# Kernel tuning notes

Hardware: AMD Instinct MI355X
Metric: run time of the kernel (lower is better)

## Reference

```python
import jax, jax.numpy as jnp
import numpy as np

SEQ, BATCH, DIM = 2048, 32, 1024


def setup_inputs() -> dict:
    key = jax.random.key(0)
    k1, k2, k3, k4, k5 = jax.random.split(key, 5)
    scale = 1.0 / np.sqrt(DIM)
    return {
        "decoder_hidden": jax.random.normal(k1, (BATCH, 1, DIM), dtype=jnp.float32),
        "encoder_out": jax.random.normal(k2, (SEQ, BATCH, DIM), dtype=jnp.float32),
        "W_enc": jax.random.normal(k3, (DIM, DIM), dtype=jnp.float32) * scale,
        "W_dec": jax.random.normal(k4, (DIM, DIM), dtype=jnp.float32) * scale,
        "V_att": jax.random.normal(k5, (1, DIM), dtype=jnp.float32) * scale,
    }


def reference(decoder_hidden, encoder_out, W_enc, W_dec, V_att):
    # encoder_out: (seq, batch, dim); decoder_hidden: (batch, 1, dim)
    # torch Linear: y = x @ W.T with W of shape (out, in)
    keys = jnp.einsum('sbd,ed->bse', encoder_out, W_enc)      # (batch, seq, dim)
    query = decoder_hidden @ W_dec.T                           # (batch, 1, dim)
    scores = jnp.tanh(keys + query)                            # (batch, seq, dim)
    logits = jnp.einsum('bsd,d->bs', scores, V_att[0])         # (batch, seq)
    alpha = jax.nn.softmax(logits, axis=1)[..., None]          # (batch, seq, 1)
    # context = alpha^T @ encoder_out_permuted -> (batch, 1, dim)
    context = jnp.einsum('bs,sbd->bd', alpha[..., 0], encoder_out)[:, None, :]
    return context, jnp.transpose(alpha, (2, 0, 1))            # (1, batch, seq)
```

## Files before the change

### kernel.cpp

```cpp
#include <hip/hip_runtime.h>
#include <hip/hip_bf16.h>
#include <math.h>

#define SEQ   2048
#define BATCH 32
#define DIM   1024
#define MROWS (SEQ*BATCH)
#define NT2   4
#define NCH   16
#define NKT   16

typedef __attribute__((ext_vector_type(8))) short short8;
typedef __attribute__((ext_vector_type(8))) unsigned short u16x8;
typedef __attribute__((ext_vector_type(4))) float f32x4;

__device__ __forceinline__ unsigned short f2bf(float f) {
  unsigned u = __builtin_bit_cast(unsigned, f);
  u += 0x7FFFu + ((u >> 16) & 1u);
  return (unsigned short)(u >> 16);
}

__device__ __forceinline__ void gl16(const unsigned short* g, unsigned short* l) {
  __builtin_amdgcn_global_load_lds(
      (const __attribute__((address_space(1))) unsigned int*)g,
      (__attribute__((address_space(3))) unsigned int*)l, 16, 0, 0);
}

__global__ __launch_bounds__(256) void conv_bf16_k(const float* __restrict__ src,
                                                   unsigned short* __restrict__ dst) {
  size_t i = ((size_t)blockIdx.x * 256 + threadIdx.x) * 8;
  float4 a = *reinterpret_cast<const float4*>(src + i);
  float4 b = *reinterpret_cast<const float4*>(src + i + 4);
  u16x8 o;
  o[0] = f2bf(a.x); o[1] = f2bf(a.y); o[2] = f2bf(a.z); o[3] = f2bf(a.w);
  o[4] = f2bf(b.x); o[5] = f2bf(b.y); o[6] = f2bf(b.z); o[7] = f2bf(b.w);
  *reinterpret_cast<u16x8*>(dst + i) = o;
}

__global__ __launch_bounds__(256) void qpart_k(const float* __restrict__ dh,
                                               const float* __restrict__ Wd,
                                               float* __restrict__ qpart) {
  const int bx = blockIdx.x;
  const int eb = bx & 3;
  const int dc = bx >> 2;
  __shared__ float ldh[BATCH][128];
  const int tid = threadIdx.x;
#pragma unroll
  for (int i = 0; i < 4; ++i) {
    int idx = tid + i * 256;
    int bb = idx >> 5, d4 = idx & 31;
    float4 v = *reinterpret_cast<const float4*>(&dh[(size_t)bb * DIM + dc * 128 + d4 * 4]);
    *reinterpret_cast<float4*>(&ldh[bb][d4 * 4]) = v;
  }
  __syncthreads();
  const int e = eb * 256 + tid;
  float acc[BATCH];
#pragma unroll
  for (int b = 0; b < BATCH; ++b) acc[b] = 0.f;
  for (int d4 = 0; d4 < 32; ++d4) {
    float4 w = *reinterpret_cast<const float4*>(&Wd[(size_t)e * DIM + dc * 128 + d4 * 4]);
#pragma unroll
    for (int b = 0; b < BATCH; ++b) {
      float4 h = *reinterpret_cast<const float4*>(&ldh[b][d4 * 4]);
      acc[b] += w.x * h.x + w.y * h.y + w.z * h.z + w.w * h.w;
    }
  }
#pragma unroll
  for (int b = 0; b < BATCH; ++b)
    qpart[((size_t)dc * BATCH + b) * DIM + e] = acc[b];
}

__global__ __launch_bounds__(256) void qred_k(const float* __restrict__ qpart,
                                              float* __restrict__ q) {
  int i = blockIdx.x * 256 + threadIdx.x;
  float s = 0.f;
#pragma unroll
  for (int dc = 0; dc < 8; ++dc) s += qpart[(size_t)dc * 32768 + i];
  q[i] = s;
}

#define BARR  __builtin_amdgcn_s_barrier()
#define LGKM0 do { asm volatile("s_waitcnt lgkmcnt(0)" ::: "memory"); \
                   __builtin_amdgcn_sched_barrier(0); } while (0)
#define VMC4  asm volatile("s_waitcnt vmcnt(4)" ::: "memory")
#define VMC0  asm volatile("s_waitcnt vmcnt(0)" ::: "memory")

#define STAGE(t, isB, h) do {                                                   \
    const unsigned short* gb_ = ((isB) ? Bbase : Abase)                         \
        + (size_t)(h) * 131072 + (size_t)(t) * 64;                              \
    char* lb_ = arena + ((t) & 1) * 65536 + ((isB) ? 32768 : 0) + (h) * 16384;  \
    gl16(gb_ + (size_t)r0 * 1024 + c0 * 8, (unsigned short*)lb_ + w * 512);     \
    gl16(gb_ + (size_t)r1 * 1024 + c1 * 8,                                      \
         (unsigned short*)(lb_ + 8192) + w * 512);                              \
  } while (0)

#define LOAD_A(d, MH) do {                                                      \
    const char* bA_ = arena + (d) * 65536;                                      \
    _Pragma("unroll") for (int i_ = 0; i_ < 4; ++i_)                            \
    _Pragma("unroll") for (int ks_ = 0; ks_ < 2; ++ks_) {                       \
      int ra_ = wr * 128 + ((MH) * 4 + i_) * 16 + fr;                           \
      int hh_ = ra_ >> 7, rr_ = ra_ & 127;                                      \
      int cb_ = (ks_ * 64 + kq * 16) ^ ((rr_ & 7) << 4);                        \
      a[i_][ks_] = *(const short8*)(bA_ + hh_ * 16384 + rr_ * 128 + cb_);       \
    } } while (0)

#define LOAD_B(d, NH) do {                                                      \
    const char* bB_ = arena + (d) * 65536 + 32768;                              \
    _Pragma("unroll") for (int j_ = 0; j_ < 2; ++j_)                            \
    _Pragma("unroll") for (int ks_ = 0; ks_ < 2; ++ks_) {                       \
      int rb_ = wc * 64 + ((NH) * 2 + j_) * 16 + fr;                            \
      int hh_ = rb_ >> 7, rr_ = rb_ & 127;                                      \
      int cb_ = (ks_ * 64 + kq * 16) ^ ((rr_ & 7) << 4);                        \
      b[NH][j_][ks_] = *(const short8*)(bB_ + hh_ * 16384 + rr_ * 128 + cb_);   \
    } } while (0)

#define DO_QUAD(MH, NH) do {                                                    \
    __builtin_amdgcn_s_setprio(1);                                              \
    _Pragma("unroll") for (int i_ = 0; i_ < 4; ++i_)                            \
    _Pragma("unroll") for (int j_ = 0; j_ < 2; ++j_)                            \
    _Pragma("unroll") for (int ks_ = 0; ks_ < 2; ++ks_)                         \
      acc[(MH) * 4 + i_][(NH) * 2 + j_] =                                       \
          __builtin_amdgcn_mfma_f32_16x16x32_bf16(                              \
              a[i_][ks_], b[NH][j_][ks_], acc[(MH) * 4 + i_][(NH) * 2 + j_],    \
              0, 0, 0);                                                         \
    __builtin_amdgcn_s_setprio(0);                                              \
  } while (0)

__global__ __launch_bounds__(512, 2) void gemm8p(const unsigned short* __restrict__ A,
                                                 const unsigned short* __restrict__ B,
                                                 const float* __restrict__ q,
                                                 const float* __restrict__ V,
                                                 float* __restrict__ lpart) {
  __shared__ __align__(16) char arena[131072];

  const int bid = blockIdx.x;
  const int wg = (bid & 7) * 128 + (bid >> 3);
  const int mt = wg >> 2, nt = wg & 3;
  const int row0 = mt * 256, col0 = nt * 256;
  const int tid = threadIdx.x;
  const int lane = tid & 63, w = tid >> 6;
  const int wr = w >> 2, wc = w & 3;
  const int fr = lane & 15, kq = lane >> 4;

  const int u0 = tid,        r0 = u0 >> 3;
  const int c0 = (u0 & 7) ^ (r0 & 7);
  const int u1 = 512 + tid,  r1 = u1 >> 3;
  const int c1 = (u1 & 7) ^ (r1 & 7);

  const unsigned short* Abase = A + (size_t)row0 * DIM;
  const unsigned short* Bbase = B + (size_t)col0 * DIM;

  f32x4 acc[8][4];
#pragma unroll
  for (int i = 0; i < 8; ++i)
#pragma unroll
    for (int j = 0; j < 4; ++j) acc[i][j] = (f32x4)(0.f);

  short8 a[4][2];
  short8 b[2][2][2];

  STAGE(0, 0, 0); STAGE(0, 0, 1); STAGE(0, 1, 0); STAGE(0, 1, 1);
  STAGE(1, 0, 0); STAGE(1, 1, 0);
  VMC0;
  BARR;

#pragma unroll 1
  for (int t2 = 0; t2 < NKT; t2 += 2) {
    const bool last = (t2 == NKT - 2);
    LOAD_A(0, 0); LOAD_B(0, 0);
    STAGE(t2 + 1, 0, 1);
    BARR; LGKM0; DO_QUAD(0, 0); BARR;
    LOAD_B(0, 1);
    STAGE(t2 + 1, 1, 1);
    BARR; LGKM0; DO_QUAD(0, 1); BARR;
    LOAD_A(0, 1);
    if (!last) STAGE(t2 + 2, 0, 0);
    BARR; LGKM0; DO_QUAD(1, 0); BARR;
    if (!last) { STAGE(t2 + 2, 1, 0); VMC4; } else { VMC0; }
    BARR; LGKM0; DO_QUAD(1, 1); BARR;
    LOAD_A(1, 0); LOAD_B(1, 0);
    if (!last) STAGE(t2 + 2, 0, 1);
    BARR; LGKM0; DO_QUAD(0, 0); BARR;
    LOAD_B(1, 1);
    if (!last) STAGE(t2 + 2, 1, 1);
    BARR; LGKM0; DO_QUAD(0, 1); BARR;
    LOAD_A(1, 1);
    if (!last) STAGE(t2 + 3, 0, 0);
    BARR; LGKM0; DO_QUAD(1, 0); BARR;
    if (!last) { STAGE(t2 + 3, 1, 0); VMC4; }
    BARR; LGKM0; DO_QUAD(1, 1); BARR;
  }

  __syncthreads();
  float* qld = (float*)arena;
  float* vld = (float*)(arena + 33280);
  float* red = (float*)(arena + 34304);
#pragma unroll
  for (int i = 0; i < 4; ++i) {
    int id = i * 512 + tid;
    int bb = id >> 6, e4 = id & 63;
    float4 v = *(const float4*)&q[(size_t)bb * DIM + col0 + e4 * 4];
    *(float4*)&qld[bb * 260 + e4 * 4] = v;
  }
  if (tid < 64) *(float4*)&vld[tid * 4] = *(const float4*)&V[col0 + tid * 4];
  __syncthreads();

#pragma unroll
  for (int mf = 0; mf < 8; ++mf) {
#pragma unroll
    for (int reg = 0; reg < 4; ++reg) {
      const int m_loc = wr * 128 + mf * 16 + kq * 4 + reg;
      const int bb = m_loc & 31;
      float val = 0.f;
#pragma unroll
      for (int nf = 0; nf < 4; ++nf) {
        const int el = wc * 64 + nf * 16 + fr;
        float x = acc[mf][nf][reg] + qld[bb * 260 + el];
        float g = __expf(2.f * x);
        float tnh = 1.f - 2.f * __builtin_amdgcn_rcpf(g + 1.f);
        val += tnh * vld[el];
      }
      val += __shfl_xor(val, 1); val += __shfl_xor(val, 2);
      val += __shfl_xor(val, 4); val += __shfl_xor(val, 8);
      if (fr == 0) red[wc * 256 + m_loc] = val;
    }
  }
  __syncthreads();
  if (tid < 256) {
    float s = red[tid] + red[256 + tid] + red[512 + tid] + red[768 + tid];
    lpart[(size_t)(row0 + tid) * NT2 + nt] = s;
  }
}

__global__ __launch_bounds__(256) void softmax_k(const float* __restrict__ lpart,
                                                 float* __restrict__ alpha) {
  const int b = blockIdx.x;
  __shared__ float lv[SEQ];
  __shared__ float sred[4];
  const int tid = threadIdx.x;
  float mx = -1e30f;
  for (int s = tid; s < SEQ; s += 256) {
    const float* p = &lpart[(size_t)(s * BATCH + b) * NT2];
    float v = p[0] + p[1] + p[2] + p[3];
    lv[s] = v;
    mx = fmaxf(mx, v);
  }
#pragma unroll
  for (int off = 32; off >= 1; off >>= 1) mx = fmaxf(mx, __shfl_xor(mx, off));
  if ((tid & 63) == 0) sred[tid >> 6] = mx;
  __syncthreads();
  mx = fmaxf(fmaxf(sred[0], sred[1]), fmaxf(sred[2], sred[3]));
  __syncthreads();
  float sm = 0.f;
  for (int s = tid; s < SEQ; s += 256) {
    float e = expf(lv[s] - mx);
    lv[s] = e;
    sm += e;
  }
#pragma unroll
  for (int off = 32; off >= 1; off >>= 1) sm += __shfl_xor(sm, off);
  if ((tid & 63) == 0) sred[tid >> 6] = sm;
  __syncthreads();
  const float inv = 1.f / (sred[0] + sred[1] + sred[2] + sred[3]);
  for (int s = tid; s < SEQ; s += 256)
    alpha[(size_t)b * SEQ + s] = lv[s] * inv;
}

__global__ __launch_bounds__(256) void ctx_part_k(const float* __restrict__ enc,
                                                  const float* __restrict__ alpha,
                                                  float* __restrict__ cpart) {
  const int blk = blockIdx.x;
  const int b = blk & 31;
  const int ch = blk >> 5;
  const int tid = threadIdx.x;
  const int s0 = ch * (SEQ / NCH);
  float4 acc = make_float4(0.f, 0.f, 0.f, 0.f);
#pragma unroll 4
  for (int i = 0; i < SEQ / NCH; ++i) {
    const int s = s0 + i;
    const float a = alpha[(size_t)b * SEQ + s];
    float4 v = *reinterpret_cast<const float4*>(
        &enc[((size_t)s * BATCH + b) * DIM + tid * 4]);
    acc.x += a * v.x; acc.y += a * v.y; acc.z += a * v.z; acc.w += a * v.w;
  }
  *reinterpret_cast<float4*>(&cpart[((size_t)ch * BATCH + b) * DIM + tid * 4]) = acc;
}

__global__ __launch_bounds__(256) void ctxred_k(const float* __restrict__ cpart,
                                                float* __restrict__ out) {
  int i = blockIdx.x * 256 + threadIdx.x;
  float s = 0.f;
#pragma unroll
  for (int ch = 0; ch < NCH; ++ch) s += cpart[(size_t)ch * 32768 + i];
  out[i] = s;
}

extern "C" void kernel_launch(void* const* d_in, const int* in_sizes, int n_in,
                              void* d_out, int out_size, void* d_ws, size_t ws_size,
                              hipStream_t stream) {
  const float* dh   = (const float*)d_in[0];
  const float* enc  = (const float*)d_in[1];
  const float* Wenc = (const float*)d_in[2];
  const float* Wdec = (const float*)d_in[3];
  const float* Vatt = (const float*)d_in[4];
  float* out = (float*)d_out;

  float* ws = (float*)d_ws;
  float* q      = ws;
  float* qpart  = ws + 32768;
  float* lpart  = ws + 294912;
  float* cpart  = ws + 819200;
  unsigned short* Wbf   = (unsigned short*)(ws + 1343488);
  unsigned short* encbf = (unsigned short*)(ws + 1867776);

  conv_bf16_k<<<dim3(512),   dim3(256), 0, stream>>>(Wenc, Wbf);
  qpart_k    <<<dim3(32),    dim3(256), 0, stream>>>(dh, Wdec, qpart);
  qred_k     <<<dim3(128),   dim3(256), 0, stream>>>(qpart, q);
  conv_bf16_k<<<dim3(32768), dim3(256), 0, stream>>>(enc, encbf);
  gemm8p     <<<dim3(1024),  dim3(512), 0, stream>>>(encbf, Wbf, q, Vatt, lpart);
  softmax_k  <<<dim3(BATCH),     dim3(256), 0, stream>>>(lpart, out + 32768);
  ctx_part_k <<<dim3(BATCH*NCH), dim3(256), 0, stream>>>(enc, out + 32768, cpart);
  ctxred_k   <<<dim3(128),       dim3(256), 0, stream>>>(cpart, out);
}
```

Before: 304.0 us.

## Software-pipeline GEMM LDS reads, use nontemporal conversion loads, bf16 context pass

The GEMM main loop is restructured with double-buffered register fragments so LDS reads for the next quadrant overlap the MFMAs of the current one. The LGKM waits are removed and vmcnt waits are finer-grained, with a new LDS row layout and staging pattern. The conversion kernel uses nontemporal loads. The context kernel now reads the bf16 copy of encoder_out instead of fp32, halving its traffic at the cost of precision, and it writes 32 partial sums instead of 16. The workspace offsets are shifted to fit the larger partial buffer.

```diff
diff --git a/kernel.cpp b/kernel.cpp
--- a/kernel.cpp
+++ b/kernel.cpp
@@ -29,11 +29,11 @@
 __global__ __launch_bounds__(256) void conv_bf16_k(const float* __restrict__ src,
                                                    unsigned short* __restrict__ dst) {
   size_t i = ((size_t)blockIdx.x * 256 + threadIdx.x) * 8;
-  float4 a = *reinterpret_cast<const float4*>(src + i);
-  float4 b = *reinterpret_cast<const float4*>(src + i + 4);
+  f32x4 a = __builtin_nontemporal_load(reinterpret_cast<const f32x4*>(src + i));
+  f32x4 b = __builtin_nontemporal_load(reinterpret_cast<const f32x4*>(src + i + 4));
   u16x8 o;
-  o[0] = f2bf(a.x); o[1] = f2bf(a.y); o[2] = f2bf(a.z); o[3] = f2bf(a.w);
-  o[4] = f2bf(b.x); o[5] = f2bf(b.y); o[6] = f2bf(b.z); o[7] = f2bf(b.w);
+  o[0] = f2bf(a[0]); o[1] = f2bf(a[1]); o[2] = f2bf(a[2]); o[3] = f2bf(a[3]);
+  o[4] = f2bf(b[0]); o[5] = f2bf(b[1]); o[6] = f2bf(b[2]); o[7] = f2bf(b[3]);
   *reinterpret_cast<u16x8*>(dst + i) = o;
 }
 
@@ -80,50 +80,54 @@
 }
 
 #define BARR  __builtin_amdgcn_s_barrier()
-#define LGKM0 do { asm volatile("s_waitcnt lgkmcnt(0)" ::: "memory"); \
-                   __builtin_amdgcn_sched_barrier(0); } while (0)
-#define VMC4  asm volatile("s_waitcnt vmcnt(4)" ::: "memory")
-#define VMC0  asm volatile("s_waitcnt vmcnt(0)" ::: "memory")
-
-#define STAGE(t, isB, h) do {                                                   \
-    const unsigned short* gb_ = ((isB) ? Bbase : Abase)                         \
-        + (size_t)(h) * 131072 + (size_t)(t) * 64;                              \
-    char* lb_ = arena + ((t) & 1) * 65536 + ((isB) ? 32768 : 0) + (h) * 16384;  \
-    gl16(gb_ + (size_t)r0 * 1024 + c0 * 8, (unsigned short*)lb_ + w * 512);     \
-    gl16(gb_ + (size_t)r1 * 1024 + c1 * 8,                                      \
-         (unsigned short*)(lb_ + 8192) + w * 512);                              \
+#define VMC(n) asm volatile("s_waitcnt vmcnt(" #n ")" ::: "memory")
+
+#define STAGE_A(t, h) do {                                                        \
+    const unsigned short* gb_ = Abase + (size_t)(t) * 64;                         \
+    char* lb_ = arena + (((t) & 1) * 65536) + (h) * 16384;                        \
+    gl16(gb_ + (size_t)(gA0 + (h) * 64) * 1024 + cSt * 8,                         \
+         (unsigned short*)lb_ + w * 512);                                         \
+    gl16(gb_ + (size_t)(gA0 + 128 + (h) * 64) * 1024 + cSt * 8,                   \
+         (unsigned short*)(lb_ + 8192) + w * 512);                                \
   } while (0)
 
-#define LOAD_A(d, MH) do {                                                      \
-    const char* bA_ = arena + (d) * 65536;                                      \
-    _Pragma("unroll") for (int i_ = 0; i_ < 4; ++i_)                            \
-    _Pragma("unroll") for (int ks_ = 0; ks_ < 2; ++ks_) {                       \
-      int ra_ = wr * 128 + ((MH) * 4 + i_) * 16 + fr;                           \
-      int hh_ = ra_ >> 7, rr_ = ra_ & 127;                                      \
-      int cb_ = (ks_ * 64 + kq * 16) ^ ((rr_ & 7) << 4);                        \
-      a[i_][ks_] = *(const short8*)(bA_ + hh_ * 16384 + rr_ * 128 + cb_);       \
+#define STAGE_B(t, h) do {                                                        \
+    const unsigned short* gb_ = Bbase + (size_t)(t) * 64;                         \
+    char* lb_ = arena + (((t) & 1) * 65536) + 32768 + (h) * 16384;                \
+    gl16(gb_ + (size_t)(gB0 + (h) * 32) * 1024 + cSt * 8,                         \
+         (unsigned short*)lb_ + w * 512);                                         \
+    gl16(gb_ + (size_t)(gB0 + 128 + (h) * 32) * 1024 + cSt * 8,                   \
+         (unsigned short*)(lb_ + 8192) + w * 512);                                \
+  } while (0)
+
+#define LOAD_A(d, MH, SET) do {                                                   \
+    const char* bA_ = arena + (d) * 65536;                                        \
+    _Pragma("unroll") for (int i_ = 0; i_ < 4; ++i_)                              \
+    _Pragma("unroll") for (int ks_ = 0; ks_ < 2; ++ks_) {                         \
+      int lrow_ = (MH) * 128 + wr * 64 + i_ * 16 + fr;                            \
+      int lc_ = (ks_ * 4 + kq) ^ (fr & 7);                                        \
+      SET[i_][ks_] = *(const short8*)(bA_ + lrow_ * 128 + lc_ * 16);              \
     } } while (0)
 
-#define LOAD_B(d, NH) do {                                                      \
-    const char* bB_ = arena + (d) * 65536 + 32768;                              \
-    _Pragma("unroll") for (int j_ = 0; j_ < 2; ++j_)                            \
-    _Pragma("unroll") for (int ks_ = 0; ks_ < 2; ++ks_) {                       \
-      int rb_ = wc * 64 + ((NH) * 2 + j_) * 16 + fr;                            \
-      int hh_ = rb_ >> 7, rr_ = rb_ & 127;                                      \
-      int cb_ = (ks_ * 64 + kq * 16) ^ ((rr_ & 7) << 4);                        \
-      b[NH][j_][ks_] = *(const short8*)(bB_ + hh_ * 16384 + rr_ * 128 + cb_);   \
+#define LOAD_B(d, NH, SET) do {                                                   \
+    const char* bB_ = arena + (d) * 65536 + 32768;                                \
+    _Pragma("unroll") for (int j_ = 0; j_ < 2; ++j_)                              \
+    _Pragma("unroll") for (int ks_ = 0; ks_ < 2; ++ks_) {                         \
+      int lrow_ = (NH) * 128 + wc * 32 + j_ * 16 + fr;                            \
+      int lc_ = (ks_ * 4 + kq) ^ (fr & 7);                                        \
+      SET[j_][ks_] = *(const short8*)(bB_ + lrow_ * 128 + lc_ * 16);              \
     } } while (0)
 
-#define DO_QUAD(MH, NH) do {                                                    \
-    __builtin_amdgcn_s_setprio(1);                                              \
-    _Pragma("unroll") for (int i_ = 0; i_ < 4; ++i_)                            \
-    _Pragma("unroll") for (int j_ = 0; j_ < 2; ++j_)                            \
-    _Pragma("unroll") for (int ks_ = 0; ks_ < 2; ++ks_)                         \
-      acc[(MH) * 4 + i_][(NH) * 2 + j_] =                                       \
-          __builtin_amdgcn_mfma_f32_16x16x32_bf16(                              \
-              a[i_][ks_], b[NH][j_][ks_], acc[(MH) * 4 + i_][(NH) * 2 + j_],    \
-              0, 0, 0);                                                         \
-    __builtin_amdgcn_s_setprio(0);                                              \
+#define DO_QUAD(ASET, BSET, MH, NH) do {                                          \
+    __builtin_amdgcn_s_setprio(1);                                                \
+    _Pragma("unroll") for (int i_ = 0; i_ < 4; ++i_)                              \
+    _Pragma("unroll") for (int j_ = 0; j_ < 2; ++j_)                              \
+    _Pragma("unroll") for (int ks_ = 0; ks_ < 2; ++ks_)                           \
+      acc[(MH) * 4 + i_][(NH) * 2 + j_] =                                         \
+          __builtin_amdgcn_mfma_f32_16x16x32_bf16(                                \
+              ASET[i_][ks_], BSET[j_][ks_], acc[(MH) * 4 + i_][(NH) * 2 + j_],    \
+              0, 0, 0);                                                           \
+    __builtin_amdgcn_s_setprio(0);                                                \
   } while (0)
 
 __global__ __launch_bounds__(512, 2) void gemm8p(const unsigned short* __restrict__ A,
@@ -142,10 +146,10 @@
   const int wr = w >> 2, wc = w & 3;
   const int fr = lane & 15, kq = lane >> 4;
 
-  const int u0 = tid,        r0 = u0 >> 3;
-  const int c0 = (u0 & 7) ^ (r0 & 7);
-  const int u1 = 512 + tid,  r1 = u1 >> 3;
-  const int c1 = (u1 & 7) ^ (r1 & 7);
+  const int lr0 = tid >> 3;
+  const int cSt = (tid & 7) ^ (lr0 & 7);
+  const int gA0 = lr0;
+  const int gB0 = (lr0 & 31) + (lr0 >> 5) * 64;
 
   const unsigned short* Abase = A + (size_t)row0 * DIM;
   const unsigned short* Bbase = B + (size_t)col0 * DIM;
@@ -156,39 +160,53 @@
 #pragma unroll
     for (int j = 0; j < 4; ++j) acc[i][j] = (f32x4)(0.f);
 
-  short8 a[4][2];
-  short8 b[2][2][2];
-
-  STAGE(0, 0, 0); STAGE(0, 0, 1); STAGE(0, 1, 0); STAGE(0, 1, 1);
-  STAGE(1, 0, 0); STAGE(1, 1, 0);
-  VMC0;
+  short8 a0[4][2], a1[4][2];
+  short8 b0[2][2], b1[2][2];
+
+  STAGE_A(0, 0); STAGE_B(0, 0); STAGE_A(0, 1); STAGE_B(0, 1);
+  STAGE_A(1, 0); STAGE_B(1, 0);
+  VMC(0);
   BARR;
+  LOAD_A(0, 0, a0); LOAD_B(0, 0, b0);
 
 #pragma unroll 1
   for (int t2 = 0; t2 < NKT; t2 += 2) {
     const bool last = (t2 == NKT - 2);
-    LOAD_A(0, 0); LOAD_B(0, 0);
-    STAGE(t2 + 1, 0, 1);
-    BARR; LGKM0; DO_QUAD(0, 0); BARR;
-    LOAD_B(0, 1);
-    STAGE(t2 + 1, 1, 1);
-    BARR; LGKM0; DO_QUAD(0, 1); BARR;
-    LOAD_A(0, 1);
-    if (!last) STAGE(t2 + 2, 0, 0);
-    BARR; LGKM0; DO_QUAD(1, 0); BARR;
-    if (!last) { STAGE(t2 + 2, 1, 0); VMC4; } else { VMC0; }
-    BARR; LGKM0; DO_QUAD(1, 1); BARR;
-    LOAD_A(1, 0); LOAD_B(1, 0);
-    if (!last) STAGE(t2 + 2, 0, 1);
-    BARR; LGKM0; DO_QUAD(0, 0); BARR;
-    LOAD_B(1, 1);
-    if (!last) STAGE(t2 + 2, 1, 1);
-    BARR; LGKM0; DO_QUAD(0, 1); BARR;
-    LOAD_A(1, 1);
-    if (!last) STAGE(t2 + 3, 0, 0);
-    BARR; LGKM0; DO_QUAD(1, 0); BARR;
-    if (!last) { STAGE(t2 + 3, 1, 0); VMC4; }
-    BARR; LGKM0; DO_QUAD(1, 1); BARR;
+    LOAD_B(0, 1, b1);
+    STAGE_A(t2 + 1, 1); STAGE_B(t2 + 1, 1);
+    DO_QUAD(a0, b0, 0, 0);
+    BARR;
+    LOAD_A(0, 1, a1);
+    DO_QUAD(a0, b1, 0, 1);
+    VMC(6); BARR;
+    LOAD_A(1, 0, a0);
+    if (!last) STAGE_A(t2 + 2, 0);
+    DO_QUAD(a1, b0, 1, 0);
+    if (last) { VMC(4); } else { VMC(6); }
+    BARR;
+    LOAD_B(1, 0, b0);
+    if (!last) STAGE_B(t2 + 2, 0);
+    DO_QUAD(a1, b1, 1, 1);
+    if (last) { VMC(0); } else { VMC(4); }
+    BARR;
+    LOAD_B(1, 1, b1);
+    if (!last) { STAGE_A(t2 + 2, 1); STAGE_B(t2 + 2, 1); }
+    DO_QUAD(a0, b0, 0, 0);
+    BARR;
+    LOAD_A(1, 1, a1);
+    DO_QUAD(a0, b1, 0, 1);
+    if (!last) VMC(6);
+    BARR;
+    LOAD_A(0, 0, a0);
+    if (!last) STAGE_A(t2 + 3, 0);
+    DO_QUAD(a1, b0, 1, 0);
+    if (!last) VMC(6);
+    BARR;
+    LOAD_B(0, 0, b0);
+    if (!last) STAGE_B(t2 + 3, 0);
+    DO_QUAD(a1, b1, 1, 1);
+    if (!last) VMC(4);
+    BARR;
   }
 
   __syncthreads();
@@ -266,24 +284,35 @@
     alpha[(size_t)b * SEQ + s] = lv[s] * inv;
 }
 
-__global__ __launch_bounds__(256) void ctx_part_k(const float* __restrict__ enc,
+__global__ __launch_bounds__(256) void ctx_part_k(const unsigned short* __restrict__ encbf,
                                                   const float* __restrict__ alpha,
                                                   float* __restrict__ cpart) {
   const int blk = blockIdx.x;
   const int b = blk & 31;
   const int ch = blk >> 5;
   const int tid = threadIdx.x;
+  const int g = tid >> 7;
+  const int d0 = (tid & 127) * 8;
   const int s0 = ch * (SEQ / NCH);
-  float4 acc = make_float4(0.f, 0.f, 0.f, 0.f);
+  float acc8[8];
+#pragma unroll
+  for (int k = 0; k < 8; ++k) acc8[k] = 0.f;
 #pragma unroll 4
-  for (int i = 0; i < SEQ / NCH; ++i) {
-    const int s = s0 + i;
+  for (int i = 0; i < SEQ / NCH; i += 2) {
+    const int s = s0 + i + g;
     const float a = alpha[(size_t)b * SEQ + s];
-    float4 v = *reinterpret_cast<const float4*>(
-        &enc[((size_t)s * BATCH + b) * DIM + tid * 4]);
-    acc.x += a * v.x; acc.y += a * v.y; acc.z += a * v.z; acc.w += a * v.w;
-  }
-  *reinterpret_cast<float4*>(&cpart[((size_t)ch * BATCH + b) * DIM + tid * 4]) = acc;
+    u16x8 v = *reinterpret_cast<const u16x8*>(&encbf[((size_t)s * BATCH + b) * DIM + d0]);
+#pragma unroll
+    for (int k = 0; k < 8; ++k) {
+      float f = __builtin_bit_cast(float, (unsigned)v[k] << 16);
+      acc8[k] += a * f;
+    }
+  }
+  size_t o = ((size_t)(ch * 2 + g) * BATCH + b) * DIM + d0;
+  float4 lo = {acc8[0], acc8[1], acc8[2], acc8[3]};
+  float4 hi = {acc8[4], acc8[5], acc8[6], acc8[7]};
+  *(float4*)&cpart[o] = lo;
+  *(float4*)&cpart[o + 4] = hi;
 }
 
 __global__ __launch_bounds__(256) void ctxred_k(const float* __restrict__ cpart,
@@ -291,7 +320,7 @@
   int i = blockIdx.x * 256 + threadIdx.x;
   float s = 0.f;
 #pragma unroll
-  for (int ch = 0; ch < NCH; ++ch) s += cpart[(size_t)ch * 32768 + i];
+  for (int ch = 0; ch < 32; ++ch) s += cpart[(size_t)ch * 32768 + i];
   out[i] = s;
 }
 
@@ -309,9 +338,9 @@
   float* q      = ws;
   float* qpart  = ws + 32768;
   float* lpart  = ws + 294912;
-  float* cpart  = ws + 819200;
-  unsigned short* Wbf   = (unsigned short*)(ws + 1343488);
-  unsigned short* encbf = (unsigned short*)(ws + 1867776);
+  float* cpart  = ws + 557056;
+  unsigned short* Wbf   = (unsigned short*)(ws + 1605632);
+  unsigned short* encbf = (unsigned short*)(ws + 2129920);
 
   conv_bf16_k<<<dim3(512),   dim3(256), 0, stream>>>(Wenc, Wbf);
   qpart_k    <<<dim3(32),    dim3(256), 0, stream>>>(dh, Wdec, qpart);
@@ -319,6 +348,6 @@
   conv_bf16_k<<<dim3(32768), dim3(256), 0, stream>>>(enc, encbf);
   gemm8p     <<<dim3(1024),  dim3(512), 0, stream>>>(encbf, Wbf, q, Vatt, lpart);
   softmax_k  <<<dim3(BATCH),     dim3(256), 0, stream>>>(lpart, out + 32768);
-  ctx_part_k <<<dim3(BATCH*NCH), dim3(256), 0, stream>>>(enc, out + 32768, cpart);
+  ctx_part_k <<<dim3(BATCH*NCH), dim3(256), 0, stream>>>(encbf, out + 32768, cpart);
   ctxred_k   <<<dim3(128),       dim3(256), 0, stream>>>(cpart, out);
 }
```

Result: slower. 368.7 us (+21.3%).
